# Kernel optimization log

Measured on AMD Instinct MI355X. Metric: run time of the kernel, lower is better.

The kernel has to match this reference:

```python
import jax, jax.numpy as jnp
import numpy as np

RANK = 8
HID = 512
EMB = 256
NODES = 100000
BS, SEQ, NN = 8, 64, 32
PE_LEN = 512


def sinusoidal_pe(length, d):
    # NOTE: original multiplies position by div_term (not divides), replicate exactly
    pos = jnp.arange(length, dtype=jnp.float32)[:, None]
    div = 10000.0 ** (jnp.arange(0, d, 2, dtype=jnp.float32) / d)
    ang = pos * div  # (length, d/2)
    return jnp.stack([jnp.sin(ang), jnp.cos(ang)], axis=-1).reshape(length, d)


def setup_inputs() -> dict:
    key = jax.random.key(0)
    ks = jax.random.split(key, 8)
    return {
        "neighbor_ids": jax.random.randint(ks[0], (BS, SEQ, NN, 2), 0, NODES),
        "node_emb": 0.02 * jax.random.normal(ks[1], (NODES, EMB), dtype=jnp.float32),
        "wl_w": 0.02 * jax.random.normal(ks[2], (RANK * HID, EMB), dtype=jnp.float32),
        "wl_b": jnp.zeros((RANK * HID,), jnp.float32),
        "wr_w": 0.02 * jax.random.normal(ks[3], (RANK * HID, EMB), dtype=jnp.float32),
        "wr_b": jnp.zeros((RANK * HID,), jnp.float32),
        "bias_base": 0.02 * jax.random.normal(ks[4], (HID,), dtype=jnp.float32),
        "node_bias": 0.02 * jax.random.normal(ks[5], (NODES, HID), dtype=jnp.float32),
        "positions": jnp.ones((PE_LEN,), jnp.float32),
    }


def reference(neighbor_ids, node_emb, wl_w, wl_b, wr_w, wr_b, bias_base, node_bias, positions):
    bs, S, nn_, _ = neighbor_ids.shape
    H = node_bias.shape[1]
    pe = sinusoidal_pe(PE_LEN, H)
    gelu = lambda x: jax.nn.gelu(x, approximate=False)  # torch nn.GELU default = exact erf
    scale = 1.0 / jnp.sqrt(jnp.float32(RANK))

    # initial energy tensor from first src node at step 0
    src0 = neighbor_ids[:, 0, 0, 0]
    e0 = gelu(gelu(node_bias[src0]) + pe[0])  # (bs, H)

    src_all = jnp.transpose(neighbor_ids[..., 0], (1, 0, 2))  # (S, bs, NN)
    tgt_all = jnp.transpose(neighbor_ids[..., 1], (1, 0, 2))

    def step(carry, xs):
        cache, loss = carry  # cache: (S, bs, H) energies of positive edges so far
        i, src, tgt = xs
        # weighted recurrent sum over previous energies, softmax over positions[:i]
        mask = jnp.arange(S) < i
        w = jax.nn.softmax(jnp.where(mask, positions[:S], -1e9))  # (S,)
        e = jnp.where(i == 0, e0, jnp.einsum('s,sbh->bh', w, cache))  # (bs, H)
        # low-rank bilinear edge transform: e @ (U^T V)/sqrt(r) == ((e U^T) V)/sqrt(r)
        U = (node_emb[src] @ wl_w.T + wl_b).reshape(bs, nn_, RANK, H)
        V = (node_emb[tgt] @ wr_w.T + wr_b).reshape(bs, nn_, RANK, H)
        proj = jnp.einsum('bh,bnrh->bnr', e, U)
        nxt = jnp.einsum('bnr,bnrh->bnh', proj, V) * scale + bias_base + node_bias[tgt]
        out = gelu(nxt + pe[i + 1])  # (bs, NN, H)
        cache = cache.at[i].set(out[:, 0])  # cache positive-edge energy
        energy = jnp.linalg.norm(out, axis=-1)  # (bs, NN)
        loss_i = -jax.nn.log_softmax(energy, axis=-1)[:, 0]  # label = 0
        return (cache, loss + loss_i.mean()), None

    cache0 = jnp.zeros((S, bs, H), node_emb.dtype)
    (_, loss), _ = jax.lax.scan(step, (cache0, jnp.float32(0.0)),
                                (jnp.arange(S), src_all, tgt_all))
    return loss / S
```

## Files before the change

kernel.cpp:

```cpp
#include <hip/hip_runtime.h>
#include <hip/hip_bf16.h>
#include <math.h>

#define S_   64
#define BS_  8
#define NN_  32
#define R_   8
#define H_   512
#define EMB_ 256
#define NT_  16384
#define KT3  2112
#define NS3  33
#define SCALE_ 0.35355339059327373f

typedef __attribute__((ext_vector_type(8))) short bf16x8;
typedef __attribute__((ext_vector_type(4))) float f32x4;
typedef __attribute__((ext_vector_type(4))) int i32x4;

__device__ __forceinline__ float gelu_exact(float x) {
    return 0.5f * x * (1.0f + erff(x * 0.70710678118654752440f));
}
__device__ __forceinline__ float gelu_fast(float x) {
    float inner = 0.7978845608028654f * fmaf(0.044715f * x, x * x, x);
    float e = __expf(2.0f * inner);
    return x * (1.0f - __builtin_amdgcn_rcpf(e + 1.0f));
}
__device__ __forceinline__ unsigned short f2bf(float v) {
    union { float f; unsigned int u; } c; c.f = v;
    unsigned int lsb = (c.u >> 16) & 1;
    c.u += 0x7fff + lsb;
    return (unsigned short)(c.u >> 16);
}
__device__ __forceinline__ int pack2bf(float a, float b) {
    return (int)((unsigned)f2bf(a) | ((unsigned)f2bf(b) << 16));
}
__device__ __forceinline__ i32x4 bf8_scale(i32x4 v, float p) {
    i32x4 out;
#pragma unroll
    for (int q = 0; q < 4; ++q) {
        unsigned u = (unsigned)v[q];
        float lo = __uint_as_float(u << 16);
        float hi = __uint_as_float(u & 0xffff0000u);
        out[q] = pack2bf(lo * p, hi * p);
    }
    return out;
}

__global__ __launch_bounds__(256) void prep_all(
        const int* __restrict__ nid, const float* __restrict__ node_emb,
        const float* __restrict__ wl_w, const float* __restrict__ wr_w,
        const float* __restrict__ node_bias,
        float* __restrict__ pe, float* __restrict__ e_all,
        unsigned short* __restrict__ Wl_bf, unsigned short* __restrict__ Wr_bf,
        unsigned short* __restrict__ E0) {
    int blk = blockIdx.x, t = threadIdx.x;
    if (blk < 4096) {
        Wl_bf[(size_t)blk * 256 + t] = f2bf(wl_w[(size_t)blk * 256 + t]);
        Wr_bf[(size_t)blk * 256 + t] = f2bf(wr_w[(size_t)blk * 256 + t]);
    } else if (blk < 4161) {
        int p = blk - 4096, j = t;
        double ex = (double)(2 * j) / 512.0;
        float divf = (float)exp(ex * 9.210340371976184);
        float ang = (float)p * divf;
        double a = (double)ang;
        pe[p * H_ + 2 * j]     = (float)sin(a);
        pe[p * H_ + 2 * j + 1] = (float)cos(a);
    } else if (blk < 4169) {
        int b = blk - 4161;
        int src0 = nid[((b * S_ + 0) * NN_ + 0) * 2 + 0];
        for (int h = t; h < H_; h += 256) {
            float pe0 = (h & 1) ? 1.0f : 0.0f;
            float g = gelu_fast(node_bias[(size_t)src0 * H_ + h]);
            e_all[b * H_ + h] = gelu_fast(g + pe0);
        }
    } else {
        int blk0 = blk - 4169;
        int row = blk0 * 16 + (t >> 4);
        int u = t & 15;
        int uv = row >> 9, pair = row & 511;
        int i = pair >> 3, b = pair & 7;
        int id = nid[((b * S_ + i) * NN_ + 0) * 2 + uv];
        const float4* src = (const float4*)(node_emb + (size_t)id * EMB_ + u * 16);
        unsigned short* dst = E0 + (size_t)row * EMB_ + u * 16;
#pragma unroll
        for (int q = 0; q < 2; ++q) {
            float4 f0 = src[2 * q], f1 = src[2 * q + 1];
            i32x4 o;
            o[0] = pack2bf(f0.x, f0.y); o[1] = pack2bf(f0.z, f0.w);
            o[2] = pack2bf(f1.x, f1.y); o[3] = pack2bf(f1.z, f1.w);
            *(i32x4*)(dst + q * 8) = o;
        }
    }
}

__global__ __launch_bounds__(256) void gemm_nt(
        const unsigned short* __restrict__ A0, const unsigned short* __restrict__ B0,
        const float* __restrict__ bias0, float* __restrict__ C0,
        const unsigned short* __restrict__ A1, const unsigned short* __restrict__ B1,
        const float* __restrict__ bias1, float* __restrict__ C1,
        int K, int ldC) {
    const unsigned short* A = blockIdx.z ? A1 : A0;
    const unsigned short* B = blockIdx.z ? B1 : B0;
    const float* bias = blockIdx.z ? bias1 : bias0;
    float* C = blockIdx.z ? C1 : C0;
    __shared__ unsigned short Als[128 * 64];
    __shared__ unsigned short Bls[128 * 64];
    int bM = blockIdx.x, bN = blockIdx.y;
    int t = threadIdx.x, w = t >> 6, l = t & 63;
    const unsigned short* Ag = A + (size_t)bM * 128 * K;
    const unsigned short* Bg = B + (size_t)bN * 128 * K;
    int srow = t >> 1, shalf = t & 1;
    size_t sgoff = (size_t)srow * K + shalf * 32;
    int nks = K >> 6;
    f32x4 acc[2][8];
#pragma unroll
    for (int m = 0; m < 2; ++m)
#pragma unroll
        for (int r = 0; r < 8; ++r) acc[m][r] = (f32x4)0.f;
    i32x4 ar[4], br[4];
    {
        const i32x4* ap = (const i32x4*)(Ag + sgoff);
        const i32x4* bp = (const i32x4*)(Bg + sgoff);
#pragma unroll
        for (int q = 0; q < 4; ++q) { ar[q] = ap[q]; br[q] = bp[q]; }
    }
    const int swz = (srow & 7) << 4;
    const int wbase = srow * 128;
    for (int ks = 0; ks < nks; ++ks) {
        __syncthreads();
#pragma unroll
        for (int q = 0; q < 4; ++q) {
            int ba = wbase + ((shalf * 64 + q * 16) ^ swz);
            *(i32x4*)((char*)Als + ba) = ar[q];
            *(i32x4*)((char*)Bls + ba) = br[q];
        }
        __syncthreads();
        if (ks + 1 < nks) {
            const i32x4* ap = (const i32x4*)(Ag + sgoff + (ks + 1) * 64);
            const i32x4* bp = (const i32x4*)(Bg + sgoff + (ks + 1) * 64);
#pragma unroll
            for (int q = 0; q < 4; ++q) { ar[q] = ap[q]; br[q] = bp[q]; }
        }
#pragma unroll
        for (int kk2 = 0; kk2 < 2; ++kk2) {
            bf16x8 af[2], bf[8];
#pragma unroll
            for (int mf = 0; mf < 2; ++mf) {
                int row = w * 32 + mf * 16 + (l & 15);
                int ba = row * 128 + (((kk2 * 64) + ((l >> 4) * 16)) ^ ((row & 7) << 4));
                af[mf] = *(const bf16x8*)((const char*)Als + ba);
            }
#pragma unroll
            for (int r = 0; r < 8; ++r) {
                int row = r * 16 + (l & 15);
                int ba = row * 128 + (((kk2 * 64) + ((l >> 4) * 16)) ^ ((row & 7) << 4));
                bf[r] = *(const bf16x8*)((const char*)Bls + ba);
            }
#pragma unroll
            for (int mf = 0; mf < 2; ++mf)
#pragma unroll
                for (int r = 0; r < 8; ++r)
                    acc[mf][r] = __builtin_amdgcn_mfma_f32_16x16x32_bf16(
                        af[mf], bf[r], acc[mf][r], 0, 0, 0);
        }
    }
    float bv[8];
#pragma unroll
    for (int nf = 0; nf < 8; ++nf)
        bv[nf] = bias ? bias[bN * 128 + nf * 16 + (l & 15)] : 0.f;
#pragma unroll
    for (int mf = 0; mf < 2; ++mf)
#pragma unroll
        for (int nf = 0; nf < 8; ++nf)
#pragma unroll
            for (int reg = 0; reg < 4; ++reg) {
                int row = bM * 128 + w * 32 + mf * 16 + (l >> 4) * 4 + reg;
                int col = bN * 128 + nf * 16 + (l & 15);
                C[(size_t)row * ldC + col] = acc[mf][nf][reg] + bv[nf];
            }
}

__global__ __launch_bounds__(256, 1) void seq_prep(
        const int* __restrict__ nid, const float* __restrict__ positions,
        const float* __restrict__ U0, const float* __restrict__ V0,
        const float* __restrict__ bias_base, const float* __restrict__ node_bias,
        const float* __restrict__ pe, float* __restrict__ e_all,
        unsigned short* __restrict__ e_bf,
        const float* __restrict__ wr_w, const float* __restrict__ wr_b,
        unsigned short* __restrict__ W3,
        const float* __restrict__ wl_w, unsigned short* __restrict__ WlT,
        const float* __restrict__ node_emb,
        unsigned short* __restrict__ Etgt, int* __restrict__ tgt_ids) {
    int blk = blockIdx.x;
    int t = threadIdx.x;
    if (blk < 8) {
        if (t >= 64) return;
        __shared__ float w_s[64], inv_s[64];
        int b = blk, l = t;
        float wv = __expf(positions[l]);
        float ps = wv;
#pragma unroll
        for (int d = 1; d < 64; d <<= 1) {
            float o = __shfl_up(ps, d, 64);
            if (l >= d) ps += o;
        }
        w_s[l] = wv;
        inv_s[l] = 1.0f / ps;

        float uA[8][8], uB[8][8];
        float nbA[8], nbB[8], peA[8], peB[8], bb[8], er[8], run[8];
        {
            size_t b0 = (size_t)b * 4096 + l * 8;
#pragma unroll
            for (int r = 0; r < 8; ++r) {
                float4 a0 = *(const float4*)&U0[b0 + r * H_];
                float4 a1 = *(const float4*)&U0[b0 + r * H_ + 4];
                uA[r][0] = a0.x; uA[r][1] = a0.y; uA[r][2] = a0.z; uA[r][3] = a0.w;
                uA[r][4] = a1.x; uA[r][5] = a1.y; uA[r][6] = a1.z; uA[r][7] = a1.w;
            }
            int tgt0 = nid[((b * S_) * NN_) * 2 + 1];
            float4 n0 = *(const float4*)&node_bias[(size_t)tgt0 * H_ + l * 8];
            float4 n1 = *(const float4*)&node_bias[(size_t)tgt0 * H_ + l * 8 + 4];
            nbA[0] = n0.x; nbA[1] = n0.y; nbA[2] = n0.z; nbA[3] = n0.w;
            nbA[4] = n1.x; nbA[5] = n1.y; nbA[6] = n1.z; nbA[7] = n1.w;
            float4 p0 = *(const float4*)&pe[H_ + l * 8];
            float4 p1 = *(const float4*)&pe[H_ + l * 8 + 4];
            peA[0] = p0.x; peA[1] = p0.y; peA[2] = p0.z; peA[3] = p0.w;
            peA[4] = p1.x; peA[5] = p1.y; peA[6] = p1.z; peA[7] = p1.w;
            float4 c0 = *(const float4*)&bias_base[l * 8];
            float4 c1 = *(const float4*)&bias_base[l * 8 + 4];
            bb[0] = c0.x; bb[1] = c0.y; bb[2] = c0.z; bb[3] = c0.w;
            bb[4] = c1.x; bb[5] = c1.y; bb[6] = c1.z; bb[7] = c1.w;
            float4 e0v = *(const float4*)&e_all[b * H_ + l * 8];
            float4 e1v = *(const float4*)&e_all[b * H_ + l * 8 + 4];
            er[0] = e0v.x; er[1] = e0v.y; er[2] = e0v.z; er[3] = e0v.w;
            er[4] = e1v.x; er[5] = e1v.y; er[6] = e1v.z; er[7] = e1v.w;
#pragma unroll
            for (int j = 0; j < 8; ++j) run[j] = 0.f;
        }

        auto step = [&](float (&uc)[8][8], float (&un)[8][8],
                        float (&nbc)[8], float (&nbn)[8],
                        float (&pc)[8], float (&pn)[8], int i) {
            if (i + 1 < S_) {
                size_t bn = ((size_t)(i + 1) * BS_ + b) * 4096 + l * 8;
#pragma unroll
                for (int r = 0; r < 8; ++r) {
                    float4 a0 = *(const float4*)&U0[bn + r * H_];
                    float4 a1 = *(const float4*)&U0[bn + r * H_ + 4];
                    un[r][0] = a0.x; un[r][1] = a0.y; un[r][2] = a0.z; un[r][3] = a0.w;
                    un[r][4] = a1.x; un[r][5] = a1.y; un[r][6] = a1.z; un[r][7] = a1.w;
                }
                int tgtn = nid[((b * S_ + i + 1) * NN_) * 2 + 1];
                float4 n0 = *(const float4*)&node_bias[(size_t)tgtn * H_ + l * 8];
                float4 n1 = *(const float4*)&node_bias[(size_t)tgtn * H_ + l * 8 + 4];
                nbn[0] = n0.x; nbn[1] = n0.y; nbn[2] = n0.z; nbn[3] = n0.w;
                nbn[4] = n1.x; nbn[5] = n1.y; nbn[6] = n1.z; nbn[7] = n1.w;
                float4 p0 = *(const float4*)&pe[(i + 2) * H_ + l * 8];
                float4 p1 = *(const float4*)&pe[(i + 2) * H_ + l * 8 + 4];
                pn[0] = p0.x; pn[1] = p0.y; pn[2] = p0.z; pn[3] = p0.w;
                pn[4] = p1.x; pn[5] = p1.y; pn[6] = p1.z; pn[7] = p1.w;
            }
            float v[8][8];
            size_t bc = ((size_t)i * BS_ + b) * 4096 + l * 8;
#pragma unroll
            for (int r = 0; r < 8; ++r) {
                float4 a0 = *(const float4*)&V0[bc + r * H_];
                float4 a1 = *(const float4*)&V0[bc + r * H_ + 4];
                v[r][0] = a0.x; v[r][1] = a0.y; v[r][2] = a0.z; v[r][3] = a0.w;
                v[r][4] = a1.x; v[r][5] = a1.y; v[r][6] = a1.z; v[r][7] = a1.w;
            }
            size_t eo = ((size_t)i * BS_ + b) * H_ + l * 8;
            *(float4*)&e_all[eo]     = make_float4(er[0], er[1], er[2], er[3]);
            *(float4*)&e_all[eo + 4] = make_float4(er[4], er[5], er[6], er[7]);
            i32x4 ep;
            ep[0] = pack2bf(er[0], er[1]); ep[1] = pack2bf(er[2], er[3]);
            ep[2] = pack2bf(er[4], er[5]); ep[3] = pack2bf(er[6], er[7]);
            *(i32x4*)&e_bf[eo] = ep;
            float pr[8];
#pragma unroll
            for (int r = 0; r < 8; ++r) {
                float p = er[0] * uc[r][0];
#pragma unroll
                for (int j = 1; j < 8; ++j) p = fmaf(er[j], uc[r][j], p);
                pr[r] = p;
            }
#pragma unroll
            for (int mask = 1; mask < 64; mask <<= 1)
#pragma unroll
                for (int r = 0; r < 8; ++r) pr[r] += __shfl_xor(pr[r], mask, 64);
            float wi = w_s[i], inv = inv_s[i];
#pragma unroll
            for (int j = 0; j < 8; ++j) {
                float nx = pr[0] * v[0][j];
#pragma unroll
                for (int r = 1; r < 8; ++r) nx = fmaf(pr[r], v[r][j], nx);
                float val = fmaf(nx, SCALE_, bb[j] + nbc[j] + pc[j]);
                float o = gelu_fast(val);
                run[j] = fmaf(wi, o, run[j]);
                er[j] = run[j] * inv;
            }
        };
        for (int i = 0; i < S_; i += 2) {
            step(uA, uB, nbA, nbB, peA, peB, i);
            step(uB, uA, nbB, nbA, peB, peA, i + 1);
        }
    } else if (blk < 8 + 512) {
        int h = blk - 8;
        for (int k = t; k < KT3; k += 256) {
            float v;
            if (k < 2048)       v = wr_w[(size_t)((k >> 8) * H_ + h) * EMB_ + (k & 255)];
            else if (k < 2056)  v = wr_b[(size_t)(k - 2048) * H_ + h];
            else                v = 0.f;
            W3[(size_t)h * KT3 + k] = f2bf(v);
        }
    } else if (blk < 8 + 512 + 256) {
        __shared__ float tile[64][65];
        int b2 = blk - 520;
        int r = b2 >> 5, hb = (b2 >> 2) & 7, cb = b2 & 3;
#pragma unroll
        for (int it = 0; it < 16; ++it) {
            int idx = it * 256 + t;
            int hl = idx >> 6, cl = idx & 63;
            tile[hl][cl] = wl_w[(size_t)(r * H_ + hb * 64 + hl) * EMB_ + cb * 64 + cl];
        }
        __syncthreads();
#pragma unroll
        for (int it = 0; it < 16; ++it) {
            int idx = it * 256 + t;
            int cl = idx >> 6, hl = idx & 63;
            WlT[(size_t)(r * EMB_ + cb * 64 + cl) * H_ + hb * 64 + hl] = f2bf(tile[hl][cl]);
        }
    } else {
        int b3 = blk - 776;
        int trip = b3 * 32 + (t >> 3);
        int u = t & 7;
        int i = trip >> 8, b = (trip >> 5) & 7, n = trip & 31;
        int id = nid[((b * S_ + i) * NN_ + n) * 2 + 1];
        if (u == 0) tgt_ids[trip] = id;
        const float4* src = (const float4*)(node_emb + (size_t)id * EMB_ + u * 32);
        unsigned short* dst = Etgt + (size_t)trip * EMB_ + u * 32;
#pragma unroll
        for (int q = 0; q < 4; ++q) {
            float4 f0 = src[2 * q], f1 = src[2 * q + 1];
            i32x4 o;
            o[0] = pack2bf(f0.x, f0.y); o[1] = pack2bf(f0.z, f0.w);
            o[2] = pack2bf(f1.x, f1.y); o[3] = pack2bf(f1.z, f1.w);
            *(i32x4*)(dst + q * 8) = o;
        }
    }
}

__global__ __launch_bounds__(512) void proj_kernel(
        const int* __restrict__ nid, const float* __restrict__ node_emb,
        const float* __restrict__ A2, const float* __restrict__ e_all,
        const float* __restrict__ wl_b, float* __restrict__ proj) {
    __shared__ float A_s[R_][EMB_];
    __shared__ float cb_s[R_];
    int pair = blockIdx.x;
    int t = threadIdx.x;
    int w = t >> 6, l = t & 63;
    int i = pair >> 3, b = pair & 7;
#pragma unroll
    for (int q = 0; q < 4; ++q) {
        int idx = q * 512 + t;
        A_s[idx >> 8][idx & 255] = A2[(size_t)pair * 2048 + idx];
    }
    {
        float p = 0.f;
#pragma unroll
        for (int k = 0; k < 8; ++k) {
            int h = l + 64 * k;
            p = fmaf(e_all[(size_t)pair * H_ + h], wl_b[(size_t)w * H_ + h], p);
        }
#pragma unroll
        for (int mask = 1; mask < 64; mask <<= 1) p += __shfl_xor(p, mask, 64);
        if (l == 0) cb_s[w] = p;
    }
    __syncthreads();
    float4 a4 = ((const float4*)A_s[w])[l];
    int id = nid[((b * S_ + i) * NN_ + 0) * 2 + 0];
    float4 em = ((const float4*)(node_emb + (size_t)id * EMB_))[l];
    for (int n = 0; n < NN_; ++n) {
        float4 cur = em;
        if (n < NN_ - 1) {
            id = nid[((b * S_ + i) * NN_ + n + 1) * 2 + 0];
            em = ((const float4*)(node_emb + (size_t)id * EMB_))[l];
        }
        float p = cur.x * a4.x + cur.y * a4.y + cur.z * a4.z + cur.w * a4.w;
#pragma unroll
        for (int off = 32; off; off >>= 1) p += __shfl_down(p, off, 64);
        if (l == 0) proj[((size_t)pair * NN_ + n) * R_ + w] = p + cb_s[w];
    }
}

__global__ __launch_bounds__(512) void gemm_v3(
        const unsigned short* __restrict__ W3, const unsigned short* __restrict__ Etgt,
        const int* __restrict__ tgt_ids, const float* __restrict__ proj,
        const float* __restrict__ bias_base, const float* __restrict__ pe,
        const float* __restrict__ node_bias, float* __restrict__ epart) {
    __shared__ unsigned short Als[128 * 64];
    __shared__ unsigned short Bls[256 * 64];
    __shared__ float proj_s[128 * R_];
    __shared__ float base_s[256];
    __shared__ float red_s[128 * 4];
    __shared__ int   tgt_s[128];
    int blkM = blockIdx.x;
    int blkN = blockIdx.y;
    int trip0 = blkM * 128;
    int i_blk = blkM >> 1;
    int t = threadIdx.x, w = t >> 6, l = t & 63;
    int wm = w >> 2, wn = w & 3;

    proj_s[t] = proj[(size_t)trip0 * R_ + t];
    proj_s[t + 512] = proj[(size_t)trip0 * R_ + t + 512];
    if (t < 256) base_s[t] = bias_base[blkN * 256 + t] + pe[(i_blk + 1) * H_ + blkN * 256 + t];
    if (t < 128) tgt_s[t] = tgt_ids[trip0 + t];
    __syncthreads();

    int srw = t >> 3, sun = t & 7;
    f32x4 acc[4][4];
#pragma unroll
    for (int m = 0; m < 4; ++m)
#pragma unroll
        for (int n = 0; n < 4; ++n) acc[m][n] = (f32x4)0.f;

    i32x4 ar[2], br[4];
#define A_LOAD(KS)                                                            \
    if ((KS) < 32) {                                                          \
        int c_ = (((KS) & 3) << 6) + (sun << 3);                              \
        _Pragma("unroll")                                                     \
        for (int q = 0; q < 2; ++q)                                           \
            ar[q] = *(const i32x4*)(Etgt + (size_t)(trip0 + q * 64 + srw) * EMB_ + c_); \
    }
#define B_LOAD(KS)                                                            \
    {                                                                         \
        _Pragma("unroll")                                                     \
        for (int q = 0; q < 4; ++q)                                           \
            br[q] = *(const i32x4*)(W3 + (size_t)(blkN * 256 + q * 64 + srw) * KT3 + (KS) * 64 + sun * 8); \
    }
#define STORE(KS)                                                             \
    {                                                                         \
        _Pragma("unroll")                                                     \
        for (int q = 0; q < 2; ++q) {                                         \
            int row = q * 64 + srw;                                           \
            i32x4 aval;                                                       \
            if ((KS) < 32) {                                                  \
                float pf = proj_s[row * R_ + ((KS) >> 2)];                    \
                aval = bf8_scale(ar[q], pf);                                  \
            } else if (sun == 0) {                                            \
                aval[0] = pack2bf(proj_s[row * R_ + 0], proj_s[row * R_ + 1]);\
                aval[1] = pack2bf(proj_s[row * R_ + 2], proj_s[row * R_ + 3]);\
                aval[2] = pack2bf(proj_s[row * R_ + 4], proj_s[row * R_ + 5]);\
                aval[3] = pack2bf(proj_s[row * R_ + 6], proj_s[row * R_ + 7]);\
            } else { aval[0] = 0; aval[1] = 0; aval[2] = 0; aval[3] = 0; }    \
            int ba = row * 128 + ((sun * 16) ^ ((row & 7) << 4));             \
            *(i32x4*)((char*)Als + ba) = aval;                                \
        }                                                                     \
        _Pragma("unroll")                                                     \
        for (int q = 0; q < 4; ++q) {                                         \
            int row = q * 64 + srw;                                           \
            int ba = row * 128 + ((sun * 16) ^ ((row & 7) << 4));             \
            *(i32x4*)((char*)Bls + ba) = br[q];                               \
        }                                                                     \
    }

    A_LOAD(0); B_LOAD(0); STORE(0);
    for (int ks = 0; ks < NS3; ++ks) {
        __syncthreads();
        if (ks + 1 < NS3) { A_LOAD(ks + 1); B_LOAD(ks + 1); }
#pragma unroll
        for (int kk2 = 0; kk2 < 2; ++kk2) {
            bf16x8 af[4], bf[4];
            int kb = kk2 * 64 + ((l >> 4) << 4);
#pragma unroll
            for (int mf = 0; mf < 4; ++mf) {
                int row = wm * 64 + mf * 16 + (l & 15);
                af[mf] = *(const bf16x8*)((const char*)Als + row * 128 + (kb ^ ((row & 7) << 4)));
            }
#pragma unroll
            for (int nf = 0; nf < 4; ++nf) {
                int row = wn * 64 + nf * 16 + (l & 15);
                bf[nf] = *(const bf16x8*)((const char*)Bls + row * 128 + (kb ^ ((row & 7) << 4)));
            }
#pragma unroll
            for (int mf = 0; mf < 4; ++mf)
#pragma unroll
                for (int nf = 0; nf < 4; ++nf)
                    acc[mf][nf] = __builtin_amdgcn_mfma_f32_16x16x32_bf16(
                        af[mf], bf[nf], acc[mf][nf], 0, 0, 0);
        }
        __syncthreads();
        if (ks + 1 < NS3) STORE(ks + 1);
    }
#undef A_LOAD
#undef B_LOAD
#undef STORE

    int hl = l & 15, lq = l >> 4;
#pragma unroll
    for (int mf = 0; mf < 4; ++mf)
#pragma unroll
        for (int reg = 0; reg < 4; ++reg) {
            int tl = wm * 64 + mf * 16 + lq * 4 + reg;
            int tgt = tgt_s[tl];
            float s = 0.f;
#pragma unroll
            for (int nf = 0; nf < 4; ++nf) {
                int hloc = wn * 64 + nf * 16 + hl;
                int h = blkN * 256 + hloc;
                float val = fmaf(acc[mf][nf][reg], SCALE_,
                                 base_s[hloc] + node_bias[(size_t)tgt * H_ + h]);
                float o = gelu_exact(val);
                s = fmaf(o, o, s);
            }
            s += __shfl_xor(s, 1, 64);
            s += __shfl_xor(s, 2, 64);
            s += __shfl_xor(s, 4, 64);
            s += __shfl_xor(s, 8, 64);
            if (hl == 0) red_s[tl * 4 + wn] = s;
        }
    __syncthreads();
    if (t < 128) {
        float s = red_s[t * 4] + red_s[t * 4 + 1] + red_s[t * 4 + 2] + red_s[t * 4 + 3];
        epart[(size_t)(trip0 + t) * 2 + blkN] = s;
    }
}

__global__ void loss_kernel(const float* __restrict__ epart, float* __restrict__ out) {
    __shared__ float red[8];
    int t = threadIdx.x;
    float en[NN_];
    float mx = -1e30f;
#pragma unroll
    for (int n = 0; n < NN_; ++n) {
        int trip = t * NN_ + n;
        en[n] = sqrtf(epart[(size_t)trip * 2] + epart[(size_t)trip * 2 + 1]);
        mx = fmaxf(mx, en[n]);
    }
    float s = 0.f;
#pragma unroll
    for (int n = 0; n < NN_; ++n) s += expf(en[n] - mx);
    float li = logf(s) + mx - en[0];
#pragma unroll
    for (int off = 32; off; off >>= 1) li += __shfl_down(li, off, 64);
    if ((t & 63) == 0) red[t >> 6] = li;
    __syncthreads();
    if (t == 0) {
        float tot = 0.f;
#pragma unroll
        for (int w = 0; w < 8; ++w) tot += red[w];
        out[0] = tot / 512.0f;
    }
}

extern "C" void kernel_launch(void* const* d_in, const int* in_sizes, int n_in,
                              void* d_out, int out_size, void* d_ws, size_t ws_size,
                              hipStream_t stream) {
    const int*   nid       = (const int*)d_in[0];
    const float* node_emb  = (const float*)d_in[1];
    const float* wl_w      = (const float*)d_in[2];
    const float* wl_b      = (const float*)d_in[3];
    const float* wr_w      = (const float*)d_in[4];
    const float* wr_b      = (const float*)d_in[5];
    const float* bias_base = (const float*)d_in[6];
    const float* node_bias = (const float*)d_in[7];
    const float* positions = (const float*)d_in[8];
    float* out = (float*)d_out;

    float* ws      = (float*)d_ws;
    float* pe      = ws;
    float* e_all   = pe + 65 * H_;
    float* U0      = e_all + 512 * H_;
    float* V0      = U0 + 512 * 4096;
    float* A2      = V0 + 512 * 4096;
    float* proj    = A2 + 512 * 2048;
    float* epart   = proj + NT_ * R_;
    unsigned short* e_bf  = (unsigned short*)(epart + 2 * NT_);
    unsigned short* W3    = e_bf + 512 * H_;
    unsigned short* Wl_bf = W3 + 512 * KT3;
    unsigned short* Wr_bf = Wl_bf + 4096 * EMB_;
    unsigned short* WlT   = Wr_bf + 4096 * EMB_;
    unsigned short* E0    = WlT + 2048 * H_;
    unsigned short* Etgt  = E0 + 1024 * EMB_;
    int* tgt_ids = (int*)(Etgt + (size_t)NT_ * EMB_);

    prep_all<<<4233, 256, 0, stream>>>(nid, node_emb, wl_w, wr_w, node_bias,
                                       pe, e_all, Wl_bf, Wr_bf, E0);
    gemm_nt<<<dim3(4, 32, 2), 256, 0, stream>>>(
        E0, Wl_bf, wl_b, U0,
        E0 + 512 * EMB_, Wr_bf, wr_b, V0, 256, 4096);
    seq_prep<<<8 + 512 + 256 + 512, 256, 0, stream>>>(
        nid, positions, U0, V0, bias_base, node_bias, pe, e_all, e_bf,
        wr_w, wr_b, W3, wl_w, WlT, node_emb, Etgt, tgt_ids);
    gemm_nt<<<dim3(4, 16, 1), 256, 0, stream>>>(
        e_bf, WlT, nullptr, A2, e_bf, WlT, nullptr, A2, 512, 2048);
    proj_kernel<<<512, 512, 0, stream>>>(nid, node_emb, A2, e_all, wl_b, proj);
    gemm_v3<<<dim3(128, 2), 512, 0, stream>>>(W3, Etgt, tgt_ids, proj,
                                              bias_base, pe, node_bias, epart);
    loss_kernel<<<1, 512, 0, stream>>>(epart, out);
}
```

Before: 204.7 us.

## Fuse bf16 conversion into UV GEMM and stream pre-swizzled W3 tiles via LDS DMA

Removes the separate prep_all kernel. The U/V GEMM now gathers node embeddings and reads fp32 weights directly, converts them to bf16 in registers, and computes the positional encoding and initial energies in extra blocks. W3 is prepacked by seq_prep into a tile image that already carries the LDS swizzle, and gemm_v3 loads it with global_load_lds into a double buffer so the B loads bypass registers and overlap compute. This saves a launch and the intermediate bf16 copies. In exchange the U/V GEMM reads fp32 operands twice per tile, and gemm_v3 uses more LDS and adds an extra barrier per k-step.

```diff
diff --git a/kernel.cpp b/kernel.cpp
--- a/kernel.cpp
+++ b/kernel.cpp
@@ -45,64 +45,135 @@
     }
     return out;
 }
-
-__global__ __launch_bounds__(256) void prep_all(
+__device__ __forceinline__ void gld_lds16(const void* g, void* l) {
+    __builtin_amdgcn_global_load_lds(
+        (const __attribute__((address_space(1))) unsigned int*)g,
+        (__attribute__((address_space(3))) unsigned int*)l, 16, 0, 0);
+}
+
+__global__ __launch_bounds__(256) void gemm_uv(
         const int* __restrict__ nid, const float* __restrict__ node_emb,
         const float* __restrict__ wl_w, const float* __restrict__ wr_w,
+        const float* __restrict__ wl_b, const float* __restrict__ wr_b,
         const float* __restrict__ node_bias,
-        float* __restrict__ pe, float* __restrict__ e_all,
-        unsigned short* __restrict__ Wl_bf, unsigned short* __restrict__ Wr_bf,
-        unsigned short* __restrict__ E0) {
-    int blk = blockIdx.x, t = threadIdx.x;
-    if (blk < 4096) {
-        Wl_bf[(size_t)blk * 256 + t] = f2bf(wl_w[(size_t)blk * 256 + t]);
-        Wr_bf[(size_t)blk * 256 + t] = f2bf(wr_w[(size_t)blk * 256 + t]);
-    } else if (blk < 4161) {
-        int p = blk - 4096, j = t;
-        double ex = (double)(2 * j) / 512.0;
-        float divf = (float)exp(ex * 9.210340371976184);
-        float ang = (float)p * divf;
-        double a = (double)ang;
-        pe[p * H_ + 2 * j]     = (float)sin(a);
-        pe[p * H_ + 2 * j + 1] = (float)cos(a);
-    } else if (blk < 4169) {
-        int b = blk - 4161;
-        int src0 = nid[((b * S_ + 0) * NN_ + 0) * 2 + 0];
-        for (int h = t; h < H_; h += 256) {
-            float pe0 = (h & 1) ? 1.0f : 0.0f;
-            float g = gelu_fast(node_bias[(size_t)src0 * H_ + h]);
-            e_all[b * H_ + h] = gelu_fast(g + pe0);
-        }
-    } else {
-        int blk0 = blk - 4169;
-        int row = blk0 * 16 + (t >> 4);
-        int u = t & 15;
-        int uv = row >> 9, pair = row & 511;
-        int i = pair >> 3, b = pair & 7;
-        int id = nid[((b * S_ + i) * NN_ + 0) * 2 + uv];
-        const float4* src = (const float4*)(node_emb + (size_t)id * EMB_ + u * 16);
-        unsigned short* dst = E0 + (size_t)row * EMB_ + u * 16;
-#pragma unroll
-        for (int q = 0; q < 2; ++q) {
-            float4 f0 = src[2 * q], f1 = src[2 * q + 1];
-            i32x4 o;
-            o[0] = pack2bf(f0.x, f0.y); o[1] = pack2bf(f0.z, f0.w);
-            o[2] = pack2bf(f1.x, f1.y); o[3] = pack2bf(f1.z, f1.w);
-            *(i32x4*)(dst + q * 8) = o;
-        }
-    }
+        float* __restrict__ U0, float* __restrict__ V0,
+        float* __restrict__ pe, float* __restrict__ e_all) {
+    int bN = blockIdx.y;
+    int t = threadIdx.x;
+    if (bN == 32) {
+        int fb = blockIdx.x + blockIdx.z * 4;
+        int pend = (fb == 7) ? 65 : fb * 8 + 8;
+        for (int p = fb * 8; p < pend; ++p) {
+            int j = t;
+            double ex = (double)(2 * j) / 512.0;
+            float divf = (float)exp(ex * 9.210340371976184);
+            float ang = (float)p * divf;
+            double a = (double)ang;
+            pe[p * H_ + 2 * j]     = (float)sin(a);
+            pe[p * H_ + 2 * j + 1] = (float)cos(a);
+        }
+        if (fb == 0) {
+            for (int x = t; x < BS_ * H_; x += 256) {
+                int b = x >> 9, h = x & 511;
+                int src0 = nid[((b * S_) * NN_) * 2];
+                float pe0 = (h & 1) ? 1.0f : 0.0f;
+                float g = gelu_fast(node_bias[(size_t)src0 * H_ + h]);
+                e_all[b * H_ + h] = gelu_fast(g + pe0);
+            }
+        }
+        return;
+    }
+    int uv = blockIdx.z;
+    const float* W  = uv ? wr_w : wl_w;
+    const float* Bb = uv ? wr_b : wl_b;
+    float* OUT = uv ? V0 : U0;
+    __shared__ unsigned short Als[128 * 64];
+    __shared__ unsigned short Bls[128 * 64];
+    int bM = blockIdx.x;
+    int w = t >> 6, l = t & 63;
+    int srow = t >> 1, shalf = t & 1;
+    int pair = bM * 128 + srow;
+    int ip = pair >> 3, bp = pair & 7;
+    int aid = nid[((bp * S_ + ip) * NN_) * 2 + uv];
+    const float* abase = node_emb + (size_t)aid * EMB_ + shalf * 32;
+    const float* bbase = W + (size_t)(bN * 128 + srow) * EMB_ + shalf * 32;
+
+    f32x4 acc[2][8];
+#pragma unroll
+    for (int m = 0; m < 2; ++m)
+#pragma unroll
+        for (int r = 0; r < 8; ++r) acc[m][r] = (f32x4)0.f;
+
+    i32x4 ar[4], br[4];
+#define UV_LOAD(KS)                                                          \
+    {                                                                        \
+        const float4* a4 = (const float4*)(abase + (KS) * 64);               \
+        const float4* b4 = (const float4*)(bbase + (KS) * 64);               \
+        _Pragma("unroll")                                                    \
+        for (int q = 0; q < 4; ++q) {                                        \
+            float4 fa0 = a4[2 * q], fa1 = a4[2 * q + 1];                     \
+            float4 fb0 = b4[2 * q], fb1 = b4[2 * q + 1];                     \
+            ar[q][0] = pack2bf(fa0.x, fa0.y); ar[q][1] = pack2bf(fa0.z, fa0.w); \
+            ar[q][2] = pack2bf(fa1.x, fa1.y); ar[q][3] = pack2bf(fa1.z, fa1.w); \
+            br[q][0] = pack2bf(fb0.x, fb0.y); br[q][1] = pack2bf(fb0.z, fb0.w); \
+            br[q][2] = pack2bf(fb1.x, fb1.y); br[q][3] = pack2bf(fb1.z, fb1.w); \
+        }                                                                    \
+    }
+    UV_LOAD(0);
+    const int swz = (srow & 7) << 4;
+    const int wbase = srow * 128;
+    for (int ks = 0; ks < 4; ++ks) {
+        __syncthreads();
+#pragma unroll
+        for (int q = 0; q < 4; ++q) {
+            int ba = wbase + ((shalf * 64 + q * 16) ^ swz);
+            *(i32x4*)((char*)Als + ba) = ar[q];
+            *(i32x4*)((char*)Bls + ba) = br[q];
+        }
+        __syncthreads();
+        if (ks + 1 < 4) UV_LOAD(ks + 1);
+#pragma unroll
+        for (int kk2 = 0; kk2 < 2; ++kk2) {
+            bf16x8 af[2], bf[8];
+#pragma unroll
+            for (int mf = 0; mf < 2; ++mf) {
+                int row = w * 32 + mf * 16 + (l & 15);
+                int ba = row * 128 + (((kk2 * 64) + ((l >> 4) * 16)) ^ ((row & 7) << 4));
+                af[mf] = *(const bf16x8*)((const char*)Als + ba);
+            }
+#pragma unroll
+            for (int r = 0; r < 8; ++r) {
+                int row = r * 16 + (l & 15);
+                int ba = row * 128 + (((kk2 * 64) + ((l >> 4) * 16)) ^ ((row & 7) << 4));
+                bf[r] = *(const bf16x8*)((const char*)Bls + ba);
+            }
+#pragma unroll
+            for (int mf = 0; mf < 2; ++mf)
+#pragma unroll
+                for (int r = 0; r < 8; ++r)
+                    acc[mf][r] = __builtin_amdgcn_mfma_f32_16x16x32_bf16(
+                        af[mf], bf[r], acc[mf][r], 0, 0, 0);
+        }
+    }
+#undef UV_LOAD
+    float bv[8];
+#pragma unroll
+    for (int nf = 0; nf < 8; ++nf) bv[nf] = Bb[bN * 128 + nf * 16 + (l & 15)];
+#pragma unroll
+    for (int mf = 0; mf < 2; ++mf)
+#pragma unroll
+        for (int nf = 0; nf < 8; ++nf)
+#pragma unroll
+            for (int reg = 0; reg < 4; ++reg) {
+                int row = bM * 128 + w * 32 + mf * 16 + (l >> 4) * 4 + reg;
+                int col = bN * 128 + nf * 16 + (l & 15);
+                OUT[(size_t)row * 4096 + col] = acc[mf][nf][reg] + bv[nf];
+            }
 }
 
 __global__ __launch_bounds__(256) void gemm_nt(
-        const unsigned short* __restrict__ A0, const unsigned short* __restrict__ B0,
-        const float* __restrict__ bias0, float* __restrict__ C0,
-        const unsigned short* __restrict__ A1, const unsigned short* __restrict__ B1,
-        const float* __restrict__ bias1, float* __restrict__ C1,
-        int K, int ldC) {
-    const unsigned short* A = blockIdx.z ? A1 : A0;
-    const unsigned short* B = blockIdx.z ? B1 : B0;
-    const float* bias = blockIdx.z ? bias1 : bias0;
-    float* C = blockIdx.z ? C1 : C0;
+        const unsigned short* __restrict__ A, const unsigned short* __restrict__ B,
+        const float* __restrict__ bias, float* __restrict__ C, int K, int ldC) {
     __shared__ unsigned short Als[128 * 64];
     __shared__ unsigned short Bls[128 * 64];
     int bM = blockIdx.x, bN = blockIdx.y;
@@ -187,7 +258,7 @@
         const float* __restrict__ pe, float* __restrict__ e_all,
         unsigned short* __restrict__ e_bf,
         const float* __restrict__ wr_w, const float* __restrict__ wr_b,
-        unsigned short* __restrict__ W3,
+        unsigned short* __restrict__ W3img,
         const float* __restrict__ wl_w, unsigned short* __restrict__ WlT,
         const float* __restrict__ node_emb,
         unsigned short* __restrict__ Etgt, int* __restrict__ tgt_ids) {
@@ -238,7 +309,6 @@
 #pragma unroll
             for (int j = 0; j < 8; ++j) run[j] = 0.f;
         }
-
         auto step = [&](float (&uc)[8][8], float (&un)[8][8],
                         float (&nbc)[8], float (&nbn)[8],
                         float (&pc)[8], float (&pn)[8], int i) {
@@ -305,18 +375,38 @@
             step(uA, uB, nbA, nbB, peA, peB, i);
             step(uB, uA, nbB, nbA, peB, peA, i + 1);
         }
-    } else if (blk < 8 + 512) {
-        int h = blk - 8;
-        for (int k = t; k < KT3; k += 256) {
-            float v;
-            if (k < 2048)       v = wr_w[(size_t)((k >> 8) * H_ + h) * EMB_ + (k & 255)];
-            else if (k < 2056)  v = wr_b[(size_t)(k - 2048) * H_ + h];
-            else                v = 0.f;
-            W3[(size_t)h * KT3 + k] = f2bf(v);
-        }
-    } else if (blk < 8 + 512 + 256) {
+    } else if (blk < 74) {
+        int blk2 = blk - 8;
+        int blkN = blk2 / 33, ks = blk2 % 33;
+        int row = t;
+        int h = blkN * 256 + row;
+        char* tbase = (char*)W3img + (size_t)blk2 * 32768;
+#pragma unroll
+        for (int slot = 0; slot < 8; ++slot) {
+            int k0 = ks * 64 + slot * 8;
+            i32x4 o;
+            if (ks < 32) {
+                const float* src = wr_w + (size_t)((k0 >> 8) * H_ + h) * EMB_ + (k0 & 255);
+                float4 f0 = *(const float4*)src;
+                float4 f1 = *(const float4*)(src + 4);
+                o[0] = pack2bf(f0.x, f0.y); o[1] = pack2bf(f0.z, f0.w);
+                o[2] = pack2bf(f1.x, f1.y); o[3] = pack2bf(f1.z, f1.w);
+            } else {
+                float vv[8];
+#pragma unroll
+                for (int j = 0; j < 8; ++j) {
+                    int k = k0 + j;
+                    vv[j] = (k < 2056) ? wr_b[(size_t)(k - 2048) * H_ + h] : 0.f;
+                }
+                o[0] = pack2bf(vv[0], vv[1]); o[1] = pack2bf(vv[2], vv[3]);
+                o[2] = pack2bf(vv[4], vv[5]); o[3] = pack2bf(vv[6], vv[7]);
+            }
+            int ba = row * 128 + ((slot * 16) ^ ((row & 7) << 4));
+            *(i32x4*)(tbase + ba) = o;
+        }
+    } else if (blk < 330) {
         __shared__ float tile[64][65];
-        int b2 = blk - 520;
+        int b2 = blk - 74;
         int r = b2 >> 5, hb = (b2 >> 2) & 7, cb = b2 & 3;
 #pragma unroll
         for (int it = 0; it < 16; ++it) {
@@ -332,7 +422,7 @@
             WlT[(size_t)(r * EMB_ + cb * 64 + cl) * H_ + hb * 64 + hl] = f2bf(tile[hl][cl]);
         }
     } else {
-        int b3 = blk - 776;
+        int b3 = blk - 330;
         int trip = b3 * 32 + (t >> 3);
         int u = t & 7;
         int i = trip >> 8, b = (trip >> 5) & 7, n = trip & 31;
@@ -395,12 +485,12 @@
 }
 
 __global__ __launch_bounds__(512) void gemm_v3(
-        const unsigned short* __restrict__ W3, const unsigned short* __restrict__ Etgt,
+        const unsigned short* __restrict__ W3img, const unsigned short* __restrict__ Etgt,
         const int* __restrict__ tgt_ids, const float* __restrict__ proj,
         const float* __restrict__ bias_base, const float* __restrict__ pe,
         const float* __restrict__ node_bias, float* __restrict__ epart) {
     __shared__ unsigned short Als[128 * 64];
-    __shared__ unsigned short Bls[256 * 64];
+    __shared__ unsigned short Bls[2][256 * 64];
     __shared__ float proj_s[128 * R_];
     __shared__ float base_s[256];
     __shared__ float red_s[128 * 4];
@@ -416,7 +506,6 @@
     proj_s[t + 512] = proj[(size_t)trip0 * R_ + t + 512];
     if (t < 256) base_s[t] = bias_base[blkN * 256 + t] + pe[(i_blk + 1) * H_ + blkN * 256 + t];
     if (t < 128) tgt_s[t] = tgt_ids[trip0 + t];
-    __syncthreads();
 
     int srw = t >> 3, sun = t & 7;
     f32x4 acc[4][4];
@@ -425,7 +514,16 @@
 #pragma unroll
         for (int n = 0; n < 4; ++n) acc[m][n] = (f32x4)0.f;
 
-    i32x4 ar[2], br[4];
+    i32x4 ar[2];
+#define ISSUE_B(KS, BUF)                                                      \
+    {                                                                         \
+        const unsigned short* gsrc = W3img + (((size_t)(blkN * 33 + (KS))) << 14) \
+                                     + (w << 9) + l * 8;                      \
+        char* lb = (char*)Bls[BUF] + (w << 10);                               \
+        _Pragma("unroll")                                                     \
+        for (int q = 0; q < 4; ++q)                                           \
+            gld_lds16(gsrc + q * 4096, lb + q * 8192);                        \
+    }
 #define A_LOAD(KS)                                                            \
     if ((KS) < 32) {                                                          \
         int c_ = (((KS) & 3) << 6) + (sun << 3);                              \
@@ -433,13 +531,7 @@
         for (int q = 0; q < 2; ++q)                                           \
             ar[q] = *(const i32x4*)(Etgt + (size_t)(trip0 + q * 64 + srw) * EMB_ + c_); \
     }
-#define B_LOAD(KS)                                                            \
-    {                                                                         \
-        _Pragma("unroll")                                                     \
-        for (int q = 0; q < 4; ++q)                                           \
-            br[q] = *(const i32x4*)(W3 + (size_t)(blkN * 256 + q * 64 + srw) * KT3 + (KS) * 64 + sun * 8); \
-    }
-#define STORE(KS)                                                             \
+#define STORE_A(KS)                                                           \
     {                                                                         \
         _Pragma("unroll")                                                     \
         for (int q = 0; q < 2; ++q) {                                         \
@@ -457,18 +549,17 @@
             int ba = row * 128 + ((sun * 16) ^ ((row & 7) << 4));             \
             *(i32x4*)((char*)Als + ba) = aval;                                \
         }                                                                     \
-        _Pragma("unroll")                                                     \
-        for (int q = 0; q < 4; ++q) {                                         \
-            int row = q * 64 + srw;                                           \
-            int ba = row * 128 + ((sun * 16) ^ ((row & 7) << 4));             \
-            *(i32x4*)((char*)Bls + ba) = br[q];                               \
-        }                                                                     \
-    }
-
-    A_LOAD(0); B_LOAD(0); STORE(0);
+    }
+
+    ISSUE_B(0, 0);
+    A_LOAD(0);
+    STORE_A(0);
+    __syncthreads();
+
     for (int ks = 0; ks < NS3; ++ks) {
-        __syncthreads();
-        if (ks + 1 < NS3) { A_LOAD(ks + 1); B_LOAD(ks + 1); }
+        int cur = ks & 1;
+        if (ks + 1 < NS3) { ISSUE_B(ks + 1, cur ^ 1); A_LOAD(ks + 1); }
+        const char* Bbase = (const char*)Bls[cur];
 #pragma unroll
         for (int kk2 = 0; kk2 < 2; ++kk2) {
             bf16x8 af[4], bf[4];
@@ -481,7 +572,7 @@
 #pragma unroll
             for (int nf = 0; nf < 4; ++nf) {
                 int row = wn * 64 + nf * 16 + (l & 15);
-                bf[nf] = *(const bf16x8*)((const char*)Bls + row * 128 + (kb ^ ((row & 7) << 4)));
+                bf[nf] = *(const bf16x8*)(Bbase + row * 128 + (kb ^ ((row & 7) << 4)));
             }
 #pragma unroll
             for (int mf = 0; mf < 4; ++mf)
@@ -491,11 +582,14 @@
                         af[mf], bf[nf], acc[mf][nf], 0, 0, 0);
         }
         __syncthreads();
-        if (ks + 1 < NS3) STORE(ks + 1);
-    }
+        if (ks + 1 < NS3) {
+            STORE_A(ks + 1);
+            __syncthreads();
+        }
+    }
+#undef ISSUE_B
 #undef A_LOAD
-#undef B_LOAD
-#undef STORE
+#undef STORE_A
 
     int hl = l & 15, lq = l >> 4;
 #pragma unroll
@@ -577,26 +671,19 @@
     float* proj    = A2 + 512 * 2048;
     float* epart   = proj + NT_ * R_;
     unsigned short* e_bf  = (unsigned short*)(epart + 2 * NT_);
-    unsigned short* W3    = e_bf + 512 * H_;
-    unsigned short* Wl_bf = W3 + 512 * KT3;
-    unsigned short* Wr_bf = Wl_bf + 4096 * EMB_;
-    unsigned short* WlT   = Wr_bf + 4096 * EMB_;
-    unsigned short* E0    = WlT + 2048 * H_;
-    unsigned short* Etgt  = E0 + 1024 * EMB_;
+    unsigned short* W3img = e_bf + 512 * H_;
+    unsigned short* WlT   = W3img + 66 * 16384;
+    unsigned short* Etgt  = WlT + 2048 * H_;
     int* tgt_ids = (int*)(Etgt + (size_t)NT_ * EMB_);
 
-    prep_all<<<4233, 256, 0, stream>>>(nid, node_emb, wl_w, wr_w, node_bias,
-                                       pe, e_all, Wl_bf, Wr_bf, E0);
-    gemm_nt<<<dim3(4, 32, 2), 256, 0, stream>>>(
-        E0, Wl_bf, wl_b, U0,
-        E0 + 512 * EMB_, Wr_bf, wr_b, V0, 256, 4096);
-    seq_prep<<<8 + 512 + 256 + 512, 256, 0, stream>>>(
+    gemm_uv<<<dim3(4, 33, 2), 256, 0, stream>>>(
+        nid, node_emb, wl_w, wr_w, wl_b, wr_b, node_bias, U0, V0, pe, e_all);
+    seq_prep<<<842, 256, 0, stream>>>(
         nid, positions, U0, V0, bias_base, node_bias, pe, e_all, e_bf,
-        wr_w, wr_b, W3, wl_w, WlT, node_emb, Etgt, tgt_ids);
-    gemm_nt<<<dim3(4, 16, 1), 256, 0, stream>>>(
-        e_bf, WlT, nullptr, A2, e_bf, WlT, nullptr, A2, 512, 2048);
+        wr_w, wr_b, W3img, wl_w, WlT, node_emb, Etgt, tgt_ids);
+    gemm_nt<<<dim3(4, 16), 256, 0, stream>>>(e_bf, WlT, nullptr, A2, 512, 2048);
     proj_kernel<<<512, 512, 0, stream>>>(nid, node_emb, A2, e_all, wl_b, proj);
-    gemm_v3<<<dim3(128, 2), 512, 0, stream>>>(W3, Etgt, tgt_ids, proj,
+    gemm_v3<<<dim3(128, 2), 512, 0, stream>>>(W3img, Etgt, tgt_ids, proj,
                                               bias_base, pe, node_bias, epart);
     loss_kernel<<<1, 512, 0, stream>>>(epart, out);
 }
```

Result: slower. 225.3 us (+10.0%).

## Fuse target-embedding gather and bf16 conversion into final bilinear GEMM

Applied to the files above, without the earlier changes.

The separate seq_prep phase that gathered target node embeddings into a bf16 staging buffer (Etgt/tgt_ids) is removed. The final GEMM now reads node_emb directly via neighbor ids, scales by proj and converts to bf16 with the hardware v_cvt_pk_bf16_f32 instruction. The GEMM is retiled to 128x128 blocks with 256 threads on a 128x4 grid, writing four partial energies per triple instead of two, which removes the cross-wave reduction in shared memory. This saves a global round trip for the gathered embeddings but does the gather and conversion redundantly across the four N-blocks, and the loop now has two barriers per k-step.

```diff
diff --git a/kernel.cpp b/kernel.cpp
--- a/kernel.cpp
+++ b/kernel.cpp
@@ -34,16 +34,10 @@
 __device__ __forceinline__ int pack2bf(float a, float b) {
     return (int)((unsigned)f2bf(a) | ((unsigned)f2bf(b) << 16));
 }
-__device__ __forceinline__ i32x4 bf8_scale(i32x4 v, float p) {
-    i32x4 out;
-#pragma unroll
-    for (int q = 0; q < 4; ++q) {
-        unsigned u = (unsigned)v[q];
-        float lo = __uint_as_float(u << 16);
-        float hi = __uint_as_float(u & 0xffff0000u);
-        out[q] = pack2bf(lo * p, hi * p);
-    }
-    return out;
+__device__ __forceinline__ int cvt_pk_bf16(float a, float b) {
+    int r;
+    asm("v_cvt_pk_bf16_f32 %0, %1, %2" : "=v"(r) : "v"(a), "v"(b));
+    return r;
 }
 
 __global__ __launch_bounds__(256) void prep_all(
@@ -188,9 +182,7 @@
         unsigned short* __restrict__ e_bf,
         const float* __restrict__ wr_w, const float* __restrict__ wr_b,
         unsigned short* __restrict__ W3,
-        const float* __restrict__ wl_w, unsigned short* __restrict__ WlT,
-        const float* __restrict__ node_emb,
-        unsigned short* __restrict__ Etgt, int* __restrict__ tgt_ids) {
+        const float* __restrict__ wl_w, unsigned short* __restrict__ WlT) {
     int blk = blockIdx.x;
     int t = threadIdx.x;
     if (blk < 8) {
@@ -238,7 +230,6 @@
 #pragma unroll
             for (int j = 0; j < 8; ++j) run[j] = 0.f;
         }
-
         auto step = [&](float (&uc)[8][8], float (&un)[8][8],
                         float (&nbc)[8], float (&nbn)[8],
                         float (&pc)[8], float (&pn)[8], int i) {
@@ -305,7 +296,7 @@
             step(uA, uB, nbA, nbB, peA, peB, i);
             step(uB, uA, nbB, nbA, peB, peA, i + 1);
         }
-    } else if (blk < 8 + 512) {
+    } else if (blk < 520) {
         int h = blk - 8;
         for (int k = t; k < KT3; k += 256) {
             float v;
@@ -314,7 +305,7 @@
             else                v = 0.f;
             W3[(size_t)h * KT3 + k] = f2bf(v);
         }
-    } else if (blk < 8 + 512 + 256) {
+    } else {
         __shared__ float tile[64][65];
         int b2 = blk - 520;
         int r = b2 >> 5, hb = (b2 >> 2) & 7, cb = b2 & 3;
@@ -330,23 +321,6 @@
             int idx = it * 256 + t;
             int cl = idx >> 6, hl = idx & 63;
             WlT[(size_t)(r * EMB_ + cb * 64 + cl) * H_ + hb * 64 + hl] = f2bf(tile[hl][cl]);
-        }
-    } else {
-        int b3 = blk - 776;
-        int trip = b3 * 32 + (t >> 3);
-        int u = t & 7;
-        int i = trip >> 8, b = (trip >> 5) & 7, n = trip & 31;
-        int id = nid[((b * S_ + i) * NN_ + n) * 2 + 1];
-        if (u == 0) tgt_ids[trip] = id;
-        const float4* src = (const float4*)(node_emb + (size_t)id * EMB_ + u * 32);
-        unsigned short* dst = Etgt + (size_t)trip * EMB_ + u * 32;
-#pragma unroll
-        for (int q = 0; q < 4; ++q) {
-            float4 f0 = src[2 * q], f1 = src[2 * q + 1];
-            i32x4 o;
-            o[0] = pack2bf(f0.x, f0.y); o[1] = pack2bf(f0.z, f0.w);
-            o[2] = pack2bf(f1.x, f1.y); o[3] = pack2bf(f1.z, f1.w);
-            *(i32x4*)(dst + q * 8) = o;
         }
     }
 }
@@ -394,121 +368,122 @@
     }
 }
 
-__global__ __launch_bounds__(512) void gemm_v3(
-        const unsigned short* __restrict__ W3, const unsigned short* __restrict__ Etgt,
-        const int* __restrict__ tgt_ids, const float* __restrict__ proj,
+__global__ __launch_bounds__(256) void gemm_v3(
+        const unsigned short* __restrict__ W3, const float* __restrict__ node_emb,
+        const int* __restrict__ nid, const float* __restrict__ proj,
         const float* __restrict__ bias_base, const float* __restrict__ pe,
         const float* __restrict__ node_bias, float* __restrict__ epart) {
     __shared__ unsigned short Als[128 * 64];
-    __shared__ unsigned short Bls[256 * 64];
+    __shared__ unsigned short Bls[128 * 64];
     __shared__ float proj_s[128 * R_];
-    __shared__ float base_s[256];
-    __shared__ float red_s[128 * 4];
+    __shared__ float base_s[128];
     __shared__ int   tgt_s[128];
     int blkM = blockIdx.x;
     int blkN = blockIdx.y;
     int trip0 = blkM * 128;
     int i_blk = blkM >> 1;
     int t = threadIdx.x, w = t >> 6, l = t & 63;
-    int wm = w >> 2, wn = w & 3;
-
-    proj_s[t] = proj[(size_t)trip0 * R_ + t];
-    proj_s[t + 512] = proj[(size_t)trip0 * R_ + t + 512];
-    if (t < 256) base_s[t] = bias_base[blkN * 256 + t] + pe[(i_blk + 1) * H_ + blkN * 256 + t];
-    if (t < 128) tgt_s[t] = tgt_ids[trip0 + t];
+
+    ((float4*)proj_s)[t] = ((const float4*)(proj + (size_t)trip0 * R_))[t];
+    if (t < 128) {
+        base_s[t] = bias_base[blkN * 128 + t] + pe[(i_blk + 1) * H_ + blkN * 128 + t];
+        int trip = trip0 + t;
+        int i = trip >> 8, b = (trip >> 5) & 7, n = trip & 31;
+        tgt_s[t] = nid[((b * S_ + i) * NN_ + n) * 2 + 1];
+    }
     __syncthreads();
 
-    int srw = t >> 3, sun = t & 7;
-    f32x4 acc[4][4];
-#pragma unroll
-    for (int m = 0; m < 4; ++m)
-#pragma unroll
-        for (int n = 0; n < 4; ++n) acc[m][n] = (f32x4)0.f;
-
-    i32x4 ar[2], br[4];
-#define A_LOAD(KS)                                                            \
-    if ((KS) < 32) {                                                          \
-        int c_ = (((KS) & 3) << 6) + (sun << 3);                              \
+    int srow = t >> 1, shalf = t & 1;
+    const float* abase = node_emb + (size_t)tgt_s[srow] * EMB_ + shalf * 32;
+    const unsigned short* bbase = W3 + (size_t)(blkN * 128 + srow) * KT3 + shalf * 32;
+    const float* prow = proj_s + srow * R_;
+
+    f32x4 acc[2][8];
+#pragma unroll
+    for (int m = 0; m < 2; ++m)
+#pragma unroll
+        for (int r = 0; r < 8; ++r) acc[m][r] = (f32x4)0.f;
+
+    i32x4 ar[4], br[4];
+#define LOAD(KS)                                                              \
+    {                                                                         \
+        if ((KS) < 32) {                                                      \
+            const float4* ap = (const float4*)(abase + (((KS) & 3) << 6));    \
+            float pf = prow[(KS) >> 2];                                       \
+            _Pragma("unroll")                                                 \
+            for (int q = 0; q < 4; ++q) {                                     \
+                float4 f0 = ap[2 * q], f1 = ap[2 * q + 1];                    \
+                ar[q][0] = cvt_pk_bf16(f0.x * pf, f0.y * pf);                 \
+                ar[q][1] = cvt_pk_bf16(f0.z * pf, f0.w * pf);                 \
+                ar[q][2] = cvt_pk_bf16(f1.x * pf, f1.y * pf);                 \
+                ar[q][3] = cvt_pk_bf16(f1.z * pf, f1.w * pf);                 \
+            }                                                                 \
+        } else {                                                              \
+            _Pragma("unroll")                                                 \
+            for (int q = 0; q < 4; ++q)                                       \
+                ar[q] = (i32x4)0;                                             \
+            if (shalf == 0) {                                                 \
+                ar[0][0] = cvt_pk_bf16(prow[0], prow[1]);                     \
+                ar[0][1] = cvt_pk_bf16(prow[2], prow[3]);                     \
+                ar[0][2] = cvt_pk_bf16(prow[4], prow[5]);                     \
+                ar[0][3] = cvt_pk_bf16(prow[6], prow[7]);                     \
+            }                                                                 \
+        }                                                                     \
+        const i32x4* bp = (const i32x4*)(bbase + (KS) * 64);                  \
         _Pragma("unroll")                                                     \
-        for (int q = 0; q < 2; ++q)                                           \
-            ar[q] = *(const i32x4*)(Etgt + (size_t)(trip0 + q * 64 + srw) * EMB_ + c_); \
-    }
-#define B_LOAD(KS)                                                            \
-    {                                                                         \
-        _Pragma("unroll")                                                     \
-        for (int q = 0; q < 4; ++q)                                           \
-            br[q] = *(const i32x4*)(W3 + (size_t)(blkN * 256 + q * 64 + srw) * KT3 + (KS) * 64 + sun * 8); \
-    }
-#define STORE(KS)                                                             \
-    {                                                                         \
-        _Pragma("unroll")                                                     \
-        for (int q = 0; q < 2; ++q) {                                         \
-            int row = q * 64 + srw;                                           \
-            i32x4 aval;                                                       \
-            if ((KS) < 32) {                                                  \
-                float pf = proj_s[row * R_ + ((KS) >> 2)];                    \
-                aval = bf8_scale(ar[q], pf);                                  \
-            } else if (sun == 0) {                                            \
-                aval[0] = pack2bf(proj_s[row * R_ + 0], proj_s[row * R_ + 1]);\
-                aval[1] = pack2bf(proj_s[row * R_ + 2], proj_s[row * R_ + 3]);\
-                aval[2] = pack2bf(proj_s[row * R_ + 4], proj_s[row * R_ + 5]);\
-                aval[3] = pack2bf(proj_s[row * R_ + 6], proj_s[row * R_ + 7]);\
-            } else { aval[0] = 0; aval[1] = 0; aval[2] = 0; aval[3] = 0; }    \
-            int ba = row * 128 + ((sun * 16) ^ ((row & 7) << 4));             \
-            *(i32x4*)((char*)Als + ba) = aval;                                \
-        }                                                                     \
-        _Pragma("unroll")                                                     \
-        for (int q = 0; q < 4; ++q) {                                         \
-            int row = q * 64 + srw;                                           \
-            int ba = row * 128 + ((sun * 16) ^ ((row & 7) << 4));             \
-            *(i32x4*)((char*)Bls + ba) = br[q];                               \
-        }                                                                     \
-    }
-
-    A_LOAD(0); B_LOAD(0); STORE(0);
+        for (int q = 0; q < 4; ++q) br[q] = bp[q];                            \
+    }
+
+    LOAD(0);
+    const int swz = (srow & 7) << 4;
+    const int wbase = srow * 128;
     for (int ks = 0; ks < NS3; ++ks) {
         __syncthreads();
-        if (ks + 1 < NS3) { A_LOAD(ks + 1); B_LOAD(ks + 1); }
+#pragma unroll
+        for (int q = 0; q < 4; ++q) {
+            int ba = wbase + ((shalf * 64 + q * 16) ^ swz);
+            *(i32x4*)((char*)Als + ba) = ar[q];
+            *(i32x4*)((char*)Bls + ba) = br[q];
+        }
+        __syncthreads();
+        if (ks + 1 < NS3) LOAD(ks + 1);
 #pragma unroll
         for (int kk2 = 0; kk2 < 2; ++kk2) {
-            bf16x8 af[4], bf[4];
-            int kb = kk2 * 64 + ((l >> 4) << 4);
-#pragma unroll
-            for (int mf = 0; mf < 4; ++mf) {
-                int row = wm * 64 + mf * 16 + (l & 15);
-                af[mf] = *(const bf16x8*)((const char*)Als + row * 128 + (kb ^ ((row & 7) << 4)));
-            }
-#pragma unroll
-            for (int nf = 0; nf < 4; ++nf) {
-                int row = wn * 64 + nf * 16 + (l & 15);
-                bf[nf] = *(const bf16x8*)((const char*)Bls + row * 128 + (kb ^ ((row & 7) << 4)));
-            }
-#pragma unroll
-            for (int mf = 0; mf < 4; ++mf)
-#pragma unroll
-                for (int nf = 0; nf < 4; ++nf)
-                    acc[mf][nf] = __builtin_amdgcn_mfma_f32_16x16x32_bf16(
-                        af[mf], bf[nf], acc[mf][nf], 0, 0, 0);
-        }
-        __syncthreads();
-        if (ks + 1 < NS3) STORE(ks + 1);
-    }
-#undef A_LOAD
-#undef B_LOAD
-#undef STORE
+            bf16x8 af[2], bf[8];
+#pragma unroll
+            for (int mf = 0; mf < 2; ++mf) {
+                int row = w * 32 + mf * 16 + (l & 15);
+                int ba = row * 128 + (((kk2 * 64) + ((l >> 4) * 16)) ^ ((row & 7) << 4));
+                af[mf] = *(const bf16x8*)((const char*)Als + ba);
+            }
+#pragma unroll
+            for (int r = 0; r < 8; ++r) {
+                int row = r * 16 + (l & 15);
+                int ba = row * 128 + (((kk2 * 64) + ((l >> 4) * 16)) ^ ((row & 7) << 4));
+                bf[r] = *(const bf16x8*)((const char*)Bls + ba);
+            }
+#pragma unroll
+            for (int mf = 0; mf < 2; ++mf)
+#pragma unroll
+                for (int r = 0; r < 8; ++r)
+                    acc[mf][r] = __builtin_amdgcn_mfma_f32_16x16x32_bf16(
+                        af[mf], bf[r], acc[mf][r], 0, 0, 0);
+        }
+    }
+#undef LOAD
 
     int hl = l & 15, lq = l >> 4;
 #pragma unroll
-    for (int mf = 0; mf < 4; ++mf)
+    for (int mf = 0; mf < 2; ++mf)
 #pragma unroll
         for (int reg = 0; reg < 4; ++reg) {
-            int tl = wm * 64 + mf * 16 + lq * 4 + reg;
+            int tl = w * 32 + mf * 16 + lq * 4 + reg;
             int tgt = tgt_s[tl];
             float s = 0.f;
 #pragma unroll
-            for (int nf = 0; nf < 4; ++nf) {
-                int hloc = wn * 64 + nf * 16 + hl;
-                int h = blkN * 256 + hloc;
+            for (int nf = 0; nf < 8; ++nf) {
+                int hloc = nf * 16 + hl;
+                int h = blkN * 128 + hloc;
                 float val = fmaf(acc[mf][nf][reg], SCALE_,
                                  base_s[hloc] + node_bias[(size_t)tgt * H_ + h]);
                 float o = gelu_exact(val);
@@ -518,13 +493,8 @@
             s += __shfl_xor(s, 2, 64);
             s += __shfl_xor(s, 4, 64);
             s += __shfl_xor(s, 8, 64);
-            if (hl == 0) red_s[tl * 4 + wn] = s;
-        }
-    __syncthreads();
-    if (t < 128) {
-        float s = red_s[t * 4] + red_s[t * 4 + 1] + red_s[t * 4 + 2] + red_s[t * 4 + 3];
-        epart[(size_t)(trip0 + t) * 2 + blkN] = s;
-    }
+            if (hl == 0) epart[(size_t)(trip0 + tl) * 4 + blkN] = s;
+        }
 }
 
 __global__ void loss_kernel(const float* __restrict__ epart, float* __restrict__ out) {
@@ -535,7 +505,8 @@
 #pragma unroll
     for (int n = 0; n < NN_; ++n) {
         int trip = t * NN_ + n;
-        en[n] = sqrtf(epart[(size_t)trip * 2] + epart[(size_t)trip * 2 + 1]);
+        float4 q = *(const float4*)&epart[(size_t)trip * 4];
+        en[n] = sqrtf(q.x + q.y + q.z + q.w);
         mx = fmaxf(mx, en[n]);
     }
     float s = 0.f;
@@ -576,27 +547,25 @@
     float* A2      = V0 + 512 * 4096;
     float* proj    = A2 + 512 * 2048;
     float* epart   = proj + NT_ * R_;
-    unsigned short* e_bf  = (unsigned short*)(epart + 2 * NT_);
+    unsigned short* e_bf  = (unsigned short*)(epart + 4 * NT_);
     unsigned short* W3    = e_bf + 512 * H_;
     unsigned short* Wl_bf = W3 + 512 * KT3;
     unsigned short* Wr_bf = Wl_bf + 4096 * EMB_;
     unsigned short* WlT   = Wr_bf + 4096 * EMB_;
     unsigned short* E0    = WlT + 2048 * H_;
-    unsigned short* Etgt  = E0 + 1024 * EMB_;
-    int* tgt_ids = (int*)(Etgt + (size_t)NT_ * EMB_);
 
     prep_all<<<4233, 256, 0, stream>>>(nid, node_emb, wl_w, wr_w, node_bias,
                                        pe, e_all, Wl_bf, Wr_bf, E0);
     gemm_nt<<<dim3(4, 32, 2), 256, 0, stream>>>(
         E0, Wl_bf, wl_b, U0,
         E0 + 512 * EMB_, Wr_bf, wr_b, V0, 256, 4096);
-    seq_prep<<<8 + 512 + 256 + 512, 256, 0, stream>>>(
+    seq_prep<<<776, 256, 0, stream>>>(
         nid, positions, U0, V0, bias_base, node_bias, pe, e_all, e_bf,
-        wr_w, wr_b, W3, wl_w, WlT, node_emb, Etgt, tgt_ids);
+        wr_w, wr_b, W3, wl_w, WlT);
     gemm_nt<<<dim3(4, 16, 1), 256, 0, stream>>>(
         e_bf, WlT, nullptr, A2, e_bf, WlT, nullptr, A2, 512, 2048);
     proj_kernel<<<512, 512, 0, stream>>>(nid, node_emb, A2, e_all, wl_b, proj);
-    gemm_v3<<<dim3(128, 2), 512, 0, stream>>>(W3, Etgt, tgt_ids, proj,
+    gemm_v3<<<dim3(128, 4), 256, 0, stream>>>(W3, node_emb, nid, proj,
                                               bias_base, pe, node_bias, epart);
     loss_kernel<<<1, 512, 0, stream>>>(epart, out);
 }
```

Measured after the change: 259.9 us. 26.9% more time.
